# Kernel optimization log

Measured on AMD Instinct MI355X. Metric: run time of the kernel, lower is better.

The kernel has to match this reference:

```python
import jax, jax.numpy as jnp
import numpy as np

B, G, S = 8, 64, 256
DIM = 41           # input_dim = enc_in*2+1
ET = 128           # embed_time = d_model+1
H = 8              # num_heads
EK = ET // H       # per-head time-embed dim
NH = 127           # nhidden = d_model


def setup_inputs() -> dict:
    key = jax.random.key(0)
    ks = jax.random.split(key, 12)
    inp = {
        "query": jax.random.normal(ks[0], (B, G, ET), jnp.float32),
        "key": jax.random.normal(ks[1], (B, S, DIM), jnp.float32),
        "value": jax.random.normal(ks[2], (B, S, DIM), jnp.float32),
        "mask": jax.random.randint(ks[3], (B, S, DIM), 0, 2).astype(jnp.float32),
        "qt": jnp.linspace(0.0, 1.0, G, dtype=jnp.float32),
        "tt": jax.random.uniform(ks[4], (B, S), jnp.float32),
        "stride_in": jnp.zeros((DIM,), jnp.float32),
        # learned params (torch Linear convention: y = x @ W.T + b; we store W already transposed)
        "Wq": jax.random.normal(ks[5], (ET, ET), jnp.float32) / np.sqrt(ET),
        "bq": jnp.zeros((ET,), jnp.float32),
        "Wk": jax.random.normal(ks[6], (DIM, ET), jnp.float32) / np.sqrt(DIM),
        "bk": jnp.zeros((ET,), jnp.float32),
        "Wo": jax.random.normal(ks[7], (DIM * H, NH), jnp.float32) / np.sqrt(DIM * H),
        "bo": jnp.zeros((NH,), jnp.float32),
        "Wr": jax.random.normal(ks[8], (DIM, DIM), jnp.float32) / np.sqrt(DIM),
        "br": jnp.zeros((DIM,), jnp.float32),
    }
    return inp


def reference(query, key, value, mask, qt, tt, stride_in, Wq, bq, Wk, bk, Wo, bo, Wr, br):
    b, s, dim = value.shape
    # per-head projections of time embeddings
    q = (query @ Wq + bq).reshape(b, -1, H, EK).transpose(0, 2, 1, 3)   # [B,H,G,EK]
    k = (key @ Wk + bk).reshape(b, -1, H, EK).transpose(0, 2, 1, 3)     # [B,H,S,EK]
    # per-channel time window half-width: sigmoid(range(stride_list))
    stride = jax.nn.sigmoid(stride_in @ Wr + br)                        # [DIM]
    # time-window mask m[b,g,s,d] = (tt in [qt[g]-stride[d], qt[g]+stride[d]]) & observed
    lo = qt[:, None] - stride[None, :]                                  # [G,DIM]
    hi = qt[:, None] + stride[None, :]                                  # [G,DIM]
    ttd = tt[:, None, :, None]                                          # [B,1,S,1]
    m = (ttd <= hi[None, :, None, :]) & (ttd >= lo[None, :, None, :])   # [B,G,S,DIM]
    m = m & (mask[:, None, :, :] != 0)
    # scaled dot-product scores, broadcast over value dim with per-dim masking
    scores = jnp.einsum('bhge,bhse->bhgs', q, k) / jnp.sqrt(jnp.float32(EK))
    scores = jnp.where(m[:, None], scores[..., None], jnp.float32(-1e9))  # [B,H,G,S,DIM]
    p_attn = jax.nn.softmax(scores, axis=-2)                              # softmax over S
    x = jnp.einsum('bhgsd,bsd->bhgd', p_attn, value)                      # [B,H,G,DIM]
    x = x.transpose(0, 2, 1, 3).reshape(b, -1, H * dim)                   # [B,G,H*DIM]
    out = x @ Wo + bo                                                     # [B,G,NH]
    return out
```

## Files before the change

kernel.cpp:

```cpp
#include <hip/hip_runtime.h>
#include <math.h>

#define B 8
#define G 64
#define S 256
#define DIM 41
#define ET 128
#define H 8
#define EK 16
#define NH 127
#define HD (H*DIM)

__global__ __launch_bounds__(256) void prep_kernel(const float* __restrict__ key,
                                                   const float* __restrict__ Wk,
                                                   const float* __restrict__ bk,
                                                   const float* __restrict__ query,
                                                   const float* __restrict__ Wq,
                                                   const float* __restrict__ bq,
                                                   const float* __restrict__ mask,
                                                   const float* __restrict__ qt,
                                                   const float* __restrict__ tt,
                                                   const float* __restrict__ stride_in,
                                                   const float* __restrict__ Wr,
                                                   const float* __restrict__ br,
                                                   float* __restrict__ kpT,
                                                   float* __restrict__ qp,
                                                   unsigned int* __restrict__ embitsT) {
    const int bid = blockIdx.x;
    const int tid = threadIdx.x;

    if (bid < 1024) {
        __shared__ float klds[2][48];
        const int half = tid >> 7;
        const int j = tid & 127;
        const int row = bid * 2 + half;
        if (j < DIM) klds[half][j] = key[row * DIM + j];
        __syncthreads();
        float acc = bk[j];
#pragma unroll
        for (int i = 0; i < DIM; ++i) acc = fmaf(klds[half][i], Wk[i * ET + j], acc);
        const int b = row >> 8, s = row & 255;
        kpT[b * 32768 + (j >> 2) * 1024 + s * 4 + (j & 3)] = acc;
    } else if (bid < 1280) {
        __shared__ float qlds[2][ET];
        const int base = (bid - 1024) * 2;
        ((float*)qlds)[tid] = query[base * ET + tid];
        __syncthreads();
        const int half = tid >> 7;
        const int j = tid & 127;
        float a0 = 0.f, a1 = 0.f, a2 = 0.f, a3 = 0.f;
#pragma unroll 8
        for (int i = 0; i < ET; i += 4) {
            a0 = fmaf(qlds[half][i + 0], Wq[(i + 0) * ET + j], a0);
            a1 = fmaf(qlds[half][i + 1], Wq[(i + 1) * ET + j], a1);
            a2 = fmaf(qlds[half][i + 2], Wq[(i + 2) * ET + j], a2);
            a3 = fmaf(qlds[half][i + 3], Wq[(i + 3) * ET + j], a3);
        }
        qp[(base + half) * ET + j] = bq[j] + ((a0 + a1) + (a2 + a3));
    } else {
        __shared__ float strd[DIM];
        const int bg = bid - 1280;
        const int b = bg >> 6, g = bg & 63;
        if (tid < DIM) {
            float a = br[tid];
            for (int i = 0; i < DIM; ++i) a = fmaf(stride_in[i], Wr[i * DIM + tid], a);
            strd[tid] = 1.0f / (1.0f + expf(-a));
        }
        const int s = tid;
        const float t = tt[b * S + s];
        const float qtg = qt[g];
        const float* mrow = mask + (size_t)(b * S + s) * DIM;
        unsigned int m0 = 0u, m1 = 0u;
#pragma unroll
        for (int d = 0; d < DIM; ++d) {
            const bool mb = (mrow[d] != 0.0f);
            if (d < 32) m0 |= ((unsigned)mb) << d;
            else        m1 |= ((unsigned)mb) << (d - 32);
        }
        __syncthreads();
        const int w = tid >> 6;
        unsigned int* outp = embitsT + (size_t)bg * (DIM * 8);
#pragma unroll
        for (int d = 0; d < DIM; ++d) {
            const float sd = strd[d];
            const float lo = qtg - sd, hi = qtg + sd;
            const unsigned int mbit = (d < 32) ? ((m0 >> d) & 1u) : ((m1 >> (d - 32)) & 1u);
            const int ok = (t >= lo) & (t <= hi) & (int)mbit;
            const unsigned long long bal = __ballot(ok);
            if ((tid & 63) == 0) {
                outp[d * 8 + 2 * w]     = (unsigned int)bal;
                outp[d * 8 + 2 * w + 1] = (unsigned int)(bal >> 32);
            }
        }
    }
}

__global__ __launch_bounds__(512) void main_kernel(const float* __restrict__ kpT,
                                                   const float* __restrict__ qp,
                                                   const unsigned int* __restrict__ embitsT,
                                                   const float* __restrict__ value,
                                                   const float* __restrict__ Wo,
                                                   const float* __restrict__ bo,
                                                   float* __restrict__ out) {
    __shared__ float se[H][S];
    __shared__ float vlds[S * DIM];
    __shared__ float qv[ET];
    __shared__ float Mb[H];
    __shared__ float xrow[HD];
    __shared__ float po[4][128];

    const int bg = blockIdx.x;
    const int b = bg >> 6;
    const int tid = threadIdx.x;

    const int hd_h = tid / DIM;
    const int hd_d = tid - hd_h * DIM;
    unsigned int ebw0 = 0, ebw1 = 0, ebw2 = 0, ebw3 = 0, ebw4 = 0, ebw5 = 0, ebw6 = 0, ebw7 = 0;
    if (tid < HD) {
        const uint4* p = reinterpret_cast<const uint4*>(embitsT + (size_t)bg * (DIM * 8) + hd_d * 8);
        const uint4 e0 = p[0], e1 = p[1];
        ebw0 = e0.x; ebw1 = e0.y; ebw2 = e0.z; ebw3 = e0.w;
        ebw4 = e1.x; ebw5 = e1.y; ebw6 = e1.z; ebw7 = e1.w;
    }

    if (tid < ET) qv[tid] = qp[(size_t)bg * ET + tid];
    for (int idx = tid; idx < S * DIM; idx += 512) vlds[idx] = value[(size_t)b * S * DIM + idx];
    __syncthreads();

    float sc[H];
    if (tid < S) {
        const int s = tid;
        const float4* kb = reinterpret_cast<const float4*>(kpT) + (size_t)b * 8192 + s;
#pragma unroll
        for (int h = 0; h < H; ++h) {
            float a = 0.f;
#pragma unroll
            for (int e4 = 0; e4 < 4; ++e4) {
                const float4 kv = kb[(h * 4 + e4) * 256];
                a = fmaf(qv[h * EK + e4 * 4 + 0], kv.x, a);
                a = fmaf(qv[h * EK + e4 * 4 + 1], kv.y, a);
                a = fmaf(qv[h * EK + e4 * 4 + 2], kv.z, a);
                a = fmaf(qv[h * EK + e4 * 4 + 3], kv.w, a);
            }
            sc[h] = a * 0.25f;
            se[h][s] = sc[h];
        }
    }
    __syncthreads();

    if (tid < S) {
        const int h = tid >> 5, j = tid & 31;
        float m = se[h][j];
#pragma unroll
        for (int k = 1; k < 8; ++k) m = fmaxf(m, se[h][j + 32 * k]);
#pragma unroll
        for (int off = 16; off; off >>= 1) m = fmaxf(m, __shfl_xor(m, off, 32));
        if (j == 0) Mb[h] = m;
    }
    __syncthreads();

    if (tid < S) {
        const int s = tid;
#pragma unroll
        for (int h = 0; h < H; ++h) se[h][s] = __expf(sc[h] - Mb[h]);
    }
    __syncthreads();

    if (tid < HD) {
        const int h = hd_h, d = hd_d;
        float Ssum = 0.f, acc = 0.f;
        const unsigned int ws[8] = {ebw0, ebw1, ebw2, ebw3, ebw4, ebw5, ebw6, ebw7};
#pragma unroll
        for (int k = 0; k < 8; ++k) {
            const unsigned int wv = ws[k];
#pragma unroll 8
            for (int i = 0; i < 32; ++i) {
                const int s = k * 32 + i;
                const float e = se[h][s];
                const float v = vlds[s * DIM + d];
                const float wgt = ((wv >> i) & 1u) ? e : 0.f;
                Ssum += wgt;
                acc = fmaf(wgt, v, acc);
            }
        }
        float r;
        if (Ssum != 0.f) {
            r = acc / Ssum;
        } else {
            float vs = 0.f;
            for (int s = 0; s < S; ++s) vs += vlds[s * DIM + d];
            r = vs * (1.0f / S);
        }
        xrow[tid] = r;
    }
    __syncthreads();

    {
        const int n = tid & 127, c = tid >> 7;
        if (n < NH) {
            const int i0 = c * 82;
            float a0 = 0.f, a1 = 0.f;
#pragma unroll 2
            for (int i = i0; i < i0 + 82; i += 2) {
                a0 = fmaf(xrow[i],     Wo[(size_t)i * NH + n],       a0);
                a1 = fmaf(xrow[i + 1], Wo[(size_t)(i + 1) * NH + n], a1);
            }
            po[c][n] = a0 + a1;
        }
    }
    __syncthreads();
    if (tid < NH) {
        out[(size_t)bg * NH + tid] = bo[tid] + ((po[0][tid] + po[1][tid]) + (po[2][tid] + po[3][tid]));
    }
}

extern "C" void kernel_launch(void* const* d_in, const int* in_sizes, int n_in,
                              void* d_out, int out_size, void* d_ws, size_t ws_size,
                              hipStream_t stream) {
    const float* query     = (const float*)d_in[0];
    const float* key       = (const float*)d_in[1];
    const float* value     = (const float*)d_in[2];
    const float* mask      = (const float*)d_in[3];
    const float* qt        = (const float*)d_in[4];
    const float* tt        = (const float*)d_in[5];
    const float* stride_in = (const float*)d_in[6];
    const float* Wq        = (const float*)d_in[7];
    const float* bq        = (const float*)d_in[8];
    const float* Wk        = (const float*)d_in[9];
    const float* bk        = (const float*)d_in[10];
    const float* Wo        = (const float*)d_in[11];
    const float* bo        = (const float*)d_in[12];
    const float* Wr        = (const float*)d_in[13];
    const float* br        = (const float*)d_in[14];
    float* out = (float*)d_out;

    float* kpT = (float*)d_ws;
    float* qp = kpT + (size_t)B * H * 4 * S * 4;
    unsigned int* embitsT = (unsigned int*)(qp + (size_t)B * G * ET);

    prep_kernel<<<1792, 256, 0, stream>>>(key, Wk, bk, query, Wq, bq, mask, qt, tt,
                                          stride_in, Wr, br, kpT, qp, embitsT);
    main_kernel<<<B * G, 512, 0, stream>>>(kpT, qp, embitsT, value, Wo, bo, out);
}
```

Baseline: 34.58 us.

## Register-tile masked softmax-value reduction and stage mask loads through shared memory

The main kernel's weighted value reduction changes from one thread per (head,dim) looping over all 256 keys to a register tile. Each thread covers 4 heads by 4 dims over a 16-key chunk, reading float4 from padded value and transposed exp buffers, and the chunks are reduced through shared memory. It also uses wave-level shuffles for the row max, drops the block to 384 threads, and stages the mask through shared memory in the prep kernel so loads coalesce. The aim is more data reuse per shared-memory load and fewer strided global reads, at the cost of more registers, an extra reduction pass, and higher LDS use.

```diff
diff --git a/kernel.cpp b/kernel.cpp
--- a/kernel.cpp
+++ b/kernel.cpp
@@ -10,6 +10,8 @@
 #define EK 16
 #define NH 127
 #define HD (H*DIM)
+#define VROW 44
+#define SEROW 12
 
 __global__ __launch_bounds__(256) void prep_kernel(const float* __restrict__ key,
                                                    const float* __restrict__ Wk,
@@ -26,39 +28,44 @@
                                                    float* __restrict__ kpT,
                                                    float* __restrict__ qp,
                                                    unsigned int* __restrict__ embitsT) {
+    __shared__ float smem[5248 + 64];
     const int bid = blockIdx.x;
     const int tid = threadIdx.x;
 
     if (bid < 1024) {
-        __shared__ float klds[2][48];
+        float* k0 = smem;
+        float* k1 = smem + 48;
         const int half = tid >> 7;
         const int j = tid & 127;
         const int row = bid * 2 + half;
-        if (j < DIM) klds[half][j] = key[row * DIM + j];
+        if (j < DIM) (half ? k1 : k0)[j] = key[row * DIM + j];
         __syncthreads();
+        const float* kr = half ? k1 : k0;
         float acc = bk[j];
 #pragma unroll
-        for (int i = 0; i < DIM; ++i) acc = fmaf(klds[half][i], Wk[i * ET + j], acc);
+        for (int i = 0; i < DIM; ++i) acc = fmaf(kr[i], Wk[i * ET + j], acc);
         const int b = row >> 8, s = row & 255;
         kpT[b * 32768 + (j >> 2) * 1024 + s * 4 + (j & 3)] = acc;
     } else if (bid < 1280) {
-        __shared__ float qlds[2][ET];
+        float* qlds = smem;
         const int base = (bid - 1024) * 2;
-        ((float*)qlds)[tid] = query[base * ET + tid];
+        qlds[tid] = query[base * ET + tid];
         __syncthreads();
         const int half = tid >> 7;
         const int j = tid & 127;
+        const float* qr = qlds + half * 128;
         float a0 = 0.f, a1 = 0.f, a2 = 0.f, a3 = 0.f;
 #pragma unroll 8
         for (int i = 0; i < ET; i += 4) {
-            a0 = fmaf(qlds[half][i + 0], Wq[(i + 0) * ET + j], a0);
-            a1 = fmaf(qlds[half][i + 1], Wq[(i + 1) * ET + j], a1);
-            a2 = fmaf(qlds[half][i + 2], Wq[(i + 2) * ET + j], a2);
-            a3 = fmaf(qlds[half][i + 3], Wq[(i + 3) * ET + j], a3);
+            a0 = fmaf(qr[i + 0], Wq[(i + 0) * ET + j], a0);
+            a1 = fmaf(qr[i + 1], Wq[(i + 1) * ET + j], a1);
+            a2 = fmaf(qr[i + 2], Wq[(i + 2) * ET + j], a2);
+            a3 = fmaf(qr[i + 3], Wq[(i + 3) * ET + j], a3);
         }
         qp[(base + half) * ET + j] = bq[j] + ((a0 + a1) + (a2 + a3));
     } else {
-        __shared__ float strd[DIM];
+        float* mlds = smem;
+        float* strd = smem + 5248;
         const int bg = bid - 1280;
         const int b = bg >> 6, g = bg & 63;
         if (tid < DIM) {
@@ -66,71 +73,81 @@
             for (int i = 0; i < DIM; ++i) a = fmaf(stride_in[i], Wr[i * DIM + tid], a);
             strd[tid] = 1.0f / (1.0f + expf(-a));
         }
-        const int s = tid;
-        const float t = tt[b * S + s];
+        __syncthreads();
         const float qtg = qt[g];
-        const float* mrow = mask + (size_t)(b * S + s) * DIM;
-        unsigned int m0 = 0u, m1 = 0u;
-#pragma unroll
-        for (int d = 0; d < DIM; ++d) {
-            const bool mb = (mrow[d] != 0.0f);
-            if (d < 32) m0 |= ((unsigned)mb) << d;
-            else        m1 |= ((unsigned)mb) << (d - 32);
-        }
-        __syncthreads();
-        const int w = tid >> 6;
-        unsigned int* outp = embitsT + (size_t)bg * (DIM * 8);
-#pragma unroll
-        for (int d = 0; d < DIM; ++d) {
-            const float sd = strd[d];
-            const float lo = qtg - sd, hi = qtg + sd;
-            const unsigned int mbit = (d < 32) ? ((m0 >> d) & 1u) : ((m1 >> (d - 32)) & 1u);
-            const int ok = (t >= lo) & (t <= hi) & (int)mbit;
-            const unsigned long long bal = __ballot(ok);
-            if ((tid & 63) == 0) {
-                outp[d * 8 + 2 * w]     = (unsigned int)bal;
-                outp[d * 8 + 2 * w + 1] = (unsigned int)(bal >> 32);
-            }
+        for (int rr = 0; rr < 2; ++rr) {
+            for (int idx = tid; idx < 5248; idx += 256)
+                mlds[idx] = mask[(size_t)b * S * DIM + rr * 5248 + idx];
+            __syncthreads();
+            if (tid < 128) {
+                const int s = rr * 128 + tid;
+                const float t = tt[b * S + s];
+                const int wv = tid >> 6;
+                const int w = rr * 2 + wv;
+                unsigned int* op = embitsT + (size_t)bg * (DIM * 8) + w * 2;
+#pragma unroll
+                for (int d = 0; d < DIM; ++d) {
+                    const float sd = strd[d];
+                    const int ok = (t >= qtg - sd) & (t <= qtg + sd) & (mlds[tid * DIM + d] != 0.0f);
+                    const unsigned long long bal = __ballot(ok);
+                    if ((tid & 63) == 0) {
+                        op[d * 8 + 0] = (unsigned int)bal;
+                        op[d * 8 + 1] = (unsigned int)(bal >> 32);
+                    }
+                }
+            }
+            __syncthreads();
         }
     }
 }
 
-__global__ __launch_bounds__(512) void main_kernel(const float* __restrict__ kpT,
+__global__ __launch_bounds__(384) void main_kernel(const float* __restrict__ kpT,
                                                    const float* __restrict__ qp,
                                                    const unsigned int* __restrict__ embitsT,
                                                    const float* __restrict__ value,
                                                    const float* __restrict__ Wo,
                                                    const float* __restrict__ bo,
                                                    float* __restrict__ out) {
-    __shared__ float se[H][S];
-    __shared__ float vlds[S * DIM];
+    __shared__ float vbuf[S * VROW];
+    __shared__ float seT[S][SEROW];
     __shared__ float qv[ET];
-    __shared__ float Mb[H];
     __shared__ float xrow[HD];
-    __shared__ float po[4][128];
+    __shared__ float po[3][128];
+    __shared__ float wmax[4][8];
+    __shared__ float Mb[8];
 
     const int bg = blockIdx.x;
     const int b = bg >> 6;
     const int tid = threadIdx.x;
 
-    const int hd_h = tid / DIM;
-    const int hd_d = tid - hd_h * DIM;
-    unsigned int ebw0 = 0, ebw1 = 0, ebw2 = 0, ebw3 = 0, ebw4 = 0, ebw5 = 0, ebw6 = 0, ebw7 = 0;
-    if (tid < HD) {
-        const uint4* p = reinterpret_cast<const uint4*>(embitsT + (size_t)bg * (DIM * 8) + hd_d * 8);
-        const uint4 e0 = p[0], e1 = p[1];
-        ebw0 = e0.x; ebw1 = e0.y; ebw2 = e0.z; ebw3 = e0.w;
-        ebw4 = e1.x; ebw5 = e1.y; ebw6 = e1.z; ebw7 = e1.w;
+    const int hh = tid / 176;
+    const int rem = tid - hh * 176;
+    const int sc = rem / 11;
+    const int d4 = rem - sc * 11;
+    unsigned int wd0 = 0, wd1 = 0, wd2 = 0, wd3 = 0;
+    if (tid < 352) {
+        const unsigned int* eb = embitsT + (size_t)bg * (DIM * 8) + (sc >> 1);
+        const int d0 = d4 * 4;
+        wd0 = (d0 + 0 < DIM) ? eb[(d0 + 0) * 8] : 0u;
+        wd1 = (d0 + 1 < DIM) ? eb[(d0 + 1) * 8] : 0u;
+        wd2 = (d0 + 2 < DIM) ? eb[(d0 + 2) * 8] : 0u;
+        wd3 = (d0 + 3 < DIM) ? eb[(d0 + 3) * 8] : 0u;
     }
 
     if (tid < ET) qv[tid] = qp[(size_t)bg * ET + tid];
-    for (int idx = tid; idx < S * DIM; idx += 512) vlds[idx] = value[(size_t)b * S * DIM + idx];
-    __syncthreads();
-
-    float sc[H];
+    for (int q = tid; q < S * 11; q += 384) {
+        const int s = q / 11, dq = q - (q / 11) * 11;
+        const float* vp = value + (size_t)b * S * DIM + s * DIM + dq * 4;
+        float4 t;
+        if (dq < 10) { t.x = vp[0]; t.y = vp[1]; t.z = vp[2]; t.w = vp[3]; }
+        else         { t.x = vp[0]; t.y = 0.f;   t.z = 0.f;   t.w = 0.f;  }
+        *reinterpret_cast<float4*>(&vbuf[s * VROW + dq * 4]) = t;
+    }
+    __syncthreads();
+
+    float sc8[H];
     if (tid < S) {
-        const int s = tid;
-        const float4* kb = reinterpret_cast<const float4*>(kpT) + (size_t)b * 8192 + s;
+        const float4* kb = reinterpret_cast<const float4*>(kpT) + (size_t)b * 8192 + tid;
 #pragma unroll
         for (int h = 0; h < H; ++h) {
             float a = 0.f;
@@ -142,53 +159,93 @@
                 a = fmaf(qv[h * EK + e4 * 4 + 2], kv.z, a);
                 a = fmaf(qv[h * EK + e4 * 4 + 3], kv.w, a);
             }
-            sc[h] = a * 0.25f;
-            se[h][s] = sc[h];
-        }
-    }
-    __syncthreads();
-
+            sc8[h] = a * 0.25f;
+        }
+#pragma unroll
+        for (int h = 0; h < H; ++h) {
+            float m = sc8[h];
+#pragma unroll
+            for (int off = 32; off; off >>= 1) m = fmaxf(m, __shfl_xor(m, off));
+            if ((tid & 63) == 0) wmax[tid >> 6][h] = m;
+        }
+    }
+    __syncthreads();
+    if (tid < H) Mb[tid] = fmaxf(fmaxf(wmax[0][tid], wmax[1][tid]),
+                                 fmaxf(wmax[2][tid], wmax[3][tid]));
+    __syncthreads();
     if (tid < S) {
-        const int h = tid >> 5, j = tid & 31;
-        float m = se[h][j];
-#pragma unroll
-        for (int k = 1; k < 8; ++k) m = fmaxf(m, se[h][j + 32 * k]);
-#pragma unroll
-        for (int off = 16; off; off >>= 1) m = fmaxf(m, __shfl_xor(m, off, 32));
-        if (j == 0) Mb[h] = m;
-    }
-    __syncthreads();
-
-    if (tid < S) {
-        const int s = tid;
-#pragma unroll
-        for (int h = 0; h < H; ++h) se[h][s] = __expf(sc[h] - Mb[h]);
+        float4 e0, e1;
+        e0.x = __expf(sc8[0] - Mb[0]); e0.y = __expf(sc8[1] - Mb[1]);
+        e0.z = __expf(sc8[2] - Mb[2]); e0.w = __expf(sc8[3] - Mb[3]);
+        e1.x = __expf(sc8[4] - Mb[4]); e1.y = __expf(sc8[5] - Mb[5]);
+        e1.z = __expf(sc8[6] - Mb[6]); e1.w = __expf(sc8[7] - Mb[7]);
+        *reinterpret_cast<float4*>(&seT[tid][0]) = e0;
+        *reinterpret_cast<float4*>(&seT[tid][4]) = e1;
+    }
+    __syncthreads();
+
+    float aS[4][4] = {{0.f}};
+    float aA[4][4] = {{0.f}};
+    if (tid < 352) {
+        const int sbase = sc * 16;
+        const int shift0 = (sc & 1) * 16;
+#pragma unroll
+        for (int i = 0; i < 16; ++i) {
+            const int s = sbase + i;
+            const float4 v = *reinterpret_cast<const float4*>(&vbuf[s * VROW + d4 * 4]);
+            const float4 e = *reinterpret_cast<const float4*>(&seT[s][hh * 4]);
+            const unsigned sh = shift0 + i;
+            const float b0 = ((wd0 >> sh) & 1u) ? 1.f : 0.f;
+            const float b1 = ((wd1 >> sh) & 1u) ? 1.f : 0.f;
+            const float b2 = ((wd2 >> sh) & 1u) ? 1.f : 0.f;
+            const float b3 = ((wd3 >> sh) & 1u) ? 1.f : 0.f;
+            const float vm0 = v.x * b0, vm1 = v.y * b1, vm2 = v.z * b2, vm3 = v.w * b3;
+            const float ee[4] = {e.x, e.y, e.z, e.w};
+#pragma unroll
+            for (int a = 0; a < 4; ++a) {
+                aA[a][0] = fmaf(ee[a], vm0, aA[a][0]);
+                aA[a][1] = fmaf(ee[a], vm1, aA[a][1]);
+                aA[a][2] = fmaf(ee[a], vm2, aA[a][2]);
+                aA[a][3] = fmaf(ee[a], vm3, aA[a][3]);
+                aS[a][0] = fmaf(ee[a], b0, aS[a][0]);
+                aS[a][1] = fmaf(ee[a], b1, aS[a][1]);
+                aS[a][2] = fmaf(ee[a], b2, aS[a][2]);
+                aS[a][3] = fmaf(ee[a], b3, aS[a][3]);
+            }
+        }
+    }
+    __syncthreads();
+
+    float* pS = vbuf;
+    float* pA = vbuf + 328 * 17;
+    if (tid < 352) {
+#pragma unroll
+        for (int a = 0; a < 4; ++a) {
+#pragma unroll
+            for (int j = 0; j < 4; ++j) {
+                const int d = d4 * 4 + j;
+                if (d < DIM) {
+                    const int hd = (hh * 4 + a) * DIM + d;
+                    pS[hd * 17 + sc] = aS[a][j];
+                    pA[hd * 17 + sc] = aA[a][j];
+                }
+            }
+        }
     }
     __syncthreads();
 
     if (tid < HD) {
-        const int h = hd_h, d = hd_d;
-        float Ssum = 0.f, acc = 0.f;
-        const unsigned int ws[8] = {ebw0, ebw1, ebw2, ebw3, ebw4, ebw5, ebw6, ebw7};
-#pragma unroll
-        for (int k = 0; k < 8; ++k) {
-            const unsigned int wv = ws[k];
-#pragma unroll 8
-            for (int i = 0; i < 32; ++i) {
-                const int s = k * 32 + i;
-                const float e = se[h][s];
-                const float v = vlds[s * DIM + d];
-                const float wgt = ((wv >> i) & 1u) ? e : 0.f;
-                Ssum += wgt;
-                acc = fmaf(wgt, v, acc);
-            }
-        }
+        float Ss = 0.f, Aa = 0.f;
+#pragma unroll
+        for (int k = 0; k < 16; ++k) { Ss += pS[tid * 17 + k]; Aa += pA[tid * 17 + k]; }
         float r;
-        if (Ssum != 0.f) {
-            r = acc / Ssum;
+        if (Ss != 0.f) {
+            r = Aa / Ss;
         } else {
+            const int d = tid % DIM;
             float vs = 0.f;
-            for (int s = 0; s < S; ++s) vs += vlds[s * DIM + d];
+            const float* vc = value + (size_t)b * S * DIM + d;
+            for (int s2 = 0; s2 < S; ++s2) vs += vc[(size_t)s2 * DIM];
             r = vs * (1.0f / S);
         }
         xrow[tid] = r;
@@ -197,11 +254,10 @@
 
     {
         const int n = tid & 127, c = tid >> 7;
+        const int i0 = c * 110, i1 = (c == 2) ? HD : (i0 + 110);
         if (n < NH) {
-            const int i0 = c * 82;
             float a0 = 0.f, a1 = 0.f;
-#pragma unroll 2
-            for (int i = i0; i < i0 + 82; i += 2) {
+            for (int i = i0; i < i1; i += 2) {
                 a0 = fmaf(xrow[i],     Wo[(size_t)i * NH + n],       a0);
                 a1 = fmaf(xrow[i + 1], Wo[(size_t)(i + 1) * NH + n], a1);
             }
@@ -209,9 +265,8 @@
         }
     }
     __syncthreads();
-    if (tid < NH) {
-        out[(size_t)bg * NH + tid] = bo[tid] + ((po[0][tid] + po[1][tid]) + (po[2][tid] + po[3][tid]));
-    }
+    if (tid < NH)
+        out[(size_t)bg * NH + tid] = bo[tid] + ((po[0][tid] + po[1][tid]) + po[2][tid]);
 }
 
 extern "C" void kernel_launch(void* const* d_in, const int* in_sizes, int n_in,
@@ -240,5 +295,5 @@
 
     prep_kernel<<<1792, 256, 0, stream>>>(key, Wk, bk, query, Wq, bq, mask, qt, tt,
                                           stride_in, Wr, br, kpT, qp, embitsT);
-    main_kernel<<<B * G, 512, 0, stream>>>(kpT, qp, embitsT, value, Wo, bo, out);
+    main_kernel<<<B * G, 384, 0, stream>>>(kpT, qp, embitsT, value, Wo, bo, out);
 }
```

Measured after the change: 52.42 us. +51.6%, slower.

## Transpose value in prep kernel and vectorize masked weighted sum via float4 LDS reads

Applied to the files above, without the earlier changes.

Adds prep blocks that write a transposed copy of value ([B,DIM,S]) to the workspace. The main kernel stages it into padded LDS rows so each thread can read four consecutive s values of both exp-scores and values as float4, replacing strided scalar LDS reads in the hot weighted-sum loop. The mask-bit blocks now stage mask rows through shared memory in two halves for coalesced global loads. The cost is an extra global round-trip for value, more shared memory in prep blocks, and half the threads idle during mask ballot.

```diff
diff --git a/kernel.cpp b/kernel.cpp
--- a/kernel.cpp
+++ b/kernel.cpp
@@ -10,6 +10,7 @@
 #define EK 16
 #define NH 127
 #define HD (H*DIM)
+#define VTROW 260
 
 __global__ __launch_bounds__(256) void prep_kernel(const float* __restrict__ key,
                                                    const float* __restrict__ Wk,
@@ -23,42 +24,49 @@
                                                    const float* __restrict__ stride_in,
                                                    const float* __restrict__ Wr,
                                                    const float* __restrict__ br,
+                                                   const float* __restrict__ value,
                                                    float* __restrict__ kpT,
                                                    float* __restrict__ qp,
-                                                   unsigned int* __restrict__ embitsT) {
+                                                   unsigned int* __restrict__ embitsT,
+                                                   float* __restrict__ vTg) {
+    __shared__ float smem[5248 + 64];
     const int bid = blockIdx.x;
     const int tid = threadIdx.x;
 
     if (bid < 1024) {
-        __shared__ float klds[2][48];
+        float* k0 = smem;
+        float* k1 = smem + 48;
         const int half = tid >> 7;
         const int j = tid & 127;
         const int row = bid * 2 + half;
-        if (j < DIM) klds[half][j] = key[row * DIM + j];
+        if (j < DIM) (half ? k1 : k0)[j] = key[row * DIM + j];
         __syncthreads();
+        const float* kr = half ? k1 : k0;
         float acc = bk[j];
 #pragma unroll
-        for (int i = 0; i < DIM; ++i) acc = fmaf(klds[half][i], Wk[i * ET + j], acc);
+        for (int i = 0; i < DIM; ++i) acc = fmaf(kr[i], Wk[i * ET + j], acc);
         const int b = row >> 8, s = row & 255;
         kpT[b * 32768 + (j >> 2) * 1024 + s * 4 + (j & 3)] = acc;
     } else if (bid < 1280) {
-        __shared__ float qlds[2][ET];
+        float* qlds = smem;
         const int base = (bid - 1024) * 2;
-        ((float*)qlds)[tid] = query[base * ET + tid];
+        qlds[tid] = query[base * ET + tid];
         __syncthreads();
         const int half = tid >> 7;
         const int j = tid & 127;
+        const float* qr = qlds + half * 128;
         float a0 = 0.f, a1 = 0.f, a2 = 0.f, a3 = 0.f;
 #pragma unroll 8
         for (int i = 0; i < ET; i += 4) {
-            a0 = fmaf(qlds[half][i + 0], Wq[(i + 0) * ET + j], a0);
-            a1 = fmaf(qlds[half][i + 1], Wq[(i + 1) * ET + j], a1);
-            a2 = fmaf(qlds[half][i + 2], Wq[(i + 2) * ET + j], a2);
-            a3 = fmaf(qlds[half][i + 3], Wq[(i + 3) * ET + j], a3);
+            a0 = fmaf(qr[i + 0], Wq[(i + 0) * ET + j], a0);
+            a1 = fmaf(qr[i + 1], Wq[(i + 1) * ET + j], a1);
+            a2 = fmaf(qr[i + 2], Wq[(i + 2) * ET + j], a2);
+            a3 = fmaf(qr[i + 3], Wq[(i + 3) * ET + j], a3);
         }
         qp[(base + half) * ET + j] = bq[j] + ((a0 + a1) + (a2 + a3));
-    } else {
-        __shared__ float strd[DIM];
+    } else if (bid < 1792) {
+        float* mlds = smem;
+        float* strd = smem + 5248;
         const int bg = bid - 1280;
         const int b = bg >> 6, g = bg & 63;
         if (tid < DIM) {
@@ -66,31 +74,36 @@
             for (int i = 0; i < DIM; ++i) a = fmaf(stride_in[i], Wr[i * DIM + tid], a);
             strd[tid] = 1.0f / (1.0f + expf(-a));
         }
-        const int s = tid;
-        const float t = tt[b * S + s];
+        __syncthreads();
         const float qtg = qt[g];
-        const float* mrow = mask + (size_t)(b * S + s) * DIM;
-        unsigned int m0 = 0u, m1 = 0u;
-#pragma unroll
-        for (int d = 0; d < DIM; ++d) {
-            const bool mb = (mrow[d] != 0.0f);
-            if (d < 32) m0 |= ((unsigned)mb) << d;
-            else        m1 |= ((unsigned)mb) << (d - 32);
-        }
-        __syncthreads();
-        const int w = tid >> 6;
-        unsigned int* outp = embitsT + (size_t)bg * (DIM * 8);
-#pragma unroll
-        for (int d = 0; d < DIM; ++d) {
-            const float sd = strd[d];
-            const float lo = qtg - sd, hi = qtg + sd;
-            const unsigned int mbit = (d < 32) ? ((m0 >> d) & 1u) : ((m1 >> (d - 32)) & 1u);
-            const int ok = (t >= lo) & (t <= hi) & (int)mbit;
-            const unsigned long long bal = __ballot(ok);
-            if ((tid & 63) == 0) {
-                outp[d * 8 + 2 * w]     = (unsigned int)bal;
-                outp[d * 8 + 2 * w + 1] = (unsigned int)(bal >> 32);
-            }
+        for (int rr = 0; rr < 2; ++rr) {
+            for (int idx = tid; idx < 5248; idx += 256)
+                mlds[idx] = mask[(size_t)b * S * DIM + rr * 5248 + idx];
+            __syncthreads();
+            if (tid < 128) {
+                const int s = rr * 128 + tid;
+                const float t = tt[b * S + s];
+                const int wv = tid >> 6;
+                const int w = rr * 2 + wv;
+                unsigned int* op = embitsT + (size_t)bg * (DIM * 8) + w * 2;
+#pragma unroll
+                for (int d = 0; d < DIM; ++d) {
+                    const float sd = strd[d];
+                    const int ok = (t >= qtg - sd) & (t <= qtg + sd) & (mlds[tid * DIM + d] != 0.0f);
+                    const unsigned long long bal = __ballot(ok);
+                    if ((tid & 63) == 0) {
+                        op[d * 8 + 0] = (unsigned int)bal;
+                        op[d * 8 + 1] = (unsigned int)(bal >> 32);
+                    }
+                }
+            }
+            __syncthreads();
+        }
+    } else {
+        const int b = bid - 1792;
+        for (int idx = tid; idx < DIM * S; idx += 256) {
+            const int d = idx >> 8, s = idx & 255;
+            vTg[(size_t)b * (DIM * S) + idx] = value[(size_t)b * S * DIM + s * DIM + d];
         }
     }
 }
@@ -98,12 +111,12 @@
 __global__ __launch_bounds__(512) void main_kernel(const float* __restrict__ kpT,
                                                    const float* __restrict__ qp,
                                                    const unsigned int* __restrict__ embitsT,
-                                                   const float* __restrict__ value,
+                                                   const float* __restrict__ vTg,
                                                    const float* __restrict__ Wo,
                                                    const float* __restrict__ bo,
                                                    float* __restrict__ out) {
+    __shared__ float vT[DIM * VTROW];
     __shared__ float se[H][S];
-    __shared__ float vlds[S * DIM];
     __shared__ float qv[ET];
     __shared__ float Mb[H];
     __shared__ float xrow[HD];
@@ -124,13 +137,15 @@
     }
 
     if (tid < ET) qv[tid] = qp[(size_t)bg * ET + tid];
-    for (int idx = tid; idx < S * DIM; idx += 512) vlds[idx] = value[(size_t)b * S * DIM + idx];
-    __syncthreads();
-
-    float sc[H];
+    for (int idx = tid; idx < DIM * S; idx += 512) {
+        const int d = idx >> 8, s = idx & 255;
+        vT[d * VTROW + s] = vTg[(size_t)b * (DIM * S) + idx];
+    }
+    __syncthreads();
+
+    float sc8[H];
     if (tid < S) {
-        const int s = tid;
-        const float4* kb = reinterpret_cast<const float4*>(kpT) + (size_t)b * 8192 + s;
+        const float4* kb = reinterpret_cast<const float4*>(kpT) + (size_t)b * 8192 + tid;
 #pragma unroll
         for (int h = 0; h < H; ++h) {
             float a = 0.f;
@@ -142,8 +157,8 @@
                 a = fmaf(qv[h * EK + e4 * 4 + 2], kv.z, a);
                 a = fmaf(qv[h * EK + e4 * 4 + 3], kv.w, a);
             }
-            sc[h] = a * 0.25f;
-            se[h][s] = sc[h];
+            sc8[h] = a * 0.25f;
+            se[h][tid] = sc8[h];
         }
     }
     __syncthreads();
@@ -160,27 +175,35 @@
     __syncthreads();
 
     if (tid < S) {
-        const int s = tid;
-#pragma unroll
-        for (int h = 0; h < H; ++h) se[h][s] = __expf(sc[h] - Mb[h]);
+#pragma unroll
+        for (int h = 0; h < H; ++h) se[h][tid] = __expf(sc8[h] - Mb[h]);
     }
     __syncthreads();
 
     if (tid < HD) {
         const int h = hd_h, d = hd_d;
+        const float* erow = &se[h][0];
+        const float* vrow = &vT[d * VTROW];
+        const unsigned int ws[8] = {ebw0, ebw1, ebw2, ebw3, ebw4, ebw5, ebw6, ebw7};
         float Ssum = 0.f, acc = 0.f;
-        const unsigned int ws[8] = {ebw0, ebw1, ebw2, ebw3, ebw4, ebw5, ebw6, ebw7};
 #pragma unroll
         for (int k = 0; k < 8; ++k) {
             const unsigned int wv = ws[k];
-#pragma unroll 8
-            for (int i = 0; i < 32; ++i) {
-                const int s = k * 32 + i;
-                const float e = se[h][s];
-                const float v = vlds[s * DIM + d];
-                const float wgt = ((wv >> i) & 1u) ? e : 0.f;
-                Ssum += wgt;
-                acc = fmaf(wgt, v, acc);
+#pragma unroll
+            for (int q = 0; q < 8; ++q) {
+                const int s0 = k * 32 + q * 4;
+                const float4 e4 = *reinterpret_cast<const float4*>(&erow[s0]);
+                const float4 v4 = *reinterpret_cast<const float4*>(&vrow[s0]);
+                const unsigned sh = q * 4;
+                const float em0 = ((wv >> (sh + 0)) & 1u) ? e4.x : 0.f;
+                const float em1 = ((wv >> (sh + 1)) & 1u) ? e4.y : 0.f;
+                const float em2 = ((wv >> (sh + 2)) & 1u) ? e4.z : 0.f;
+                const float em3 = ((wv >> (sh + 3)) & 1u) ? e4.w : 0.f;
+                Ssum += em0 + em1 + em2 + em3;
+                acc = fmaf(em0, v4.x, acc);
+                acc = fmaf(em1, v4.y, acc);
+                acc = fmaf(em2, v4.z, acc);
+                acc = fmaf(em3, v4.w, acc);
             }
         }
         float r;
@@ -188,7 +211,7 @@
             r = acc / Ssum;
         } else {
             float vs = 0.f;
-            for (int s = 0; s < S; ++s) vs += vlds[s * DIM + d];
+            for (int s2 = 0; s2 < S; ++s2) vs += vrow[s2];
             r = vs * (1.0f / S);
         }
         xrow[tid] = r;
@@ -209,9 +232,8 @@
         }
     }
     __syncthreads();
-    if (tid < NH) {
+    if (tid < NH)
         out[(size_t)bg * NH + tid] = bo[tid] + ((po[0][tid] + po[1][tid]) + (po[2][tid] + po[3][tid]));
-    }
 }
 
 extern "C" void kernel_launch(void* const* d_in, const int* in_sizes, int n_in,
@@ -237,8 +259,9 @@
     float* kpT = (float*)d_ws;
     float* qp = kpT + (size_t)B * H * 4 * S * 4;
     unsigned int* embitsT = (unsigned int*)(qp + (size_t)B * G * ET);
-
-    prep_kernel<<<1792, 256, 0, stream>>>(key, Wk, bk, query, Wq, bq, mask, qt, tt,
-                                          stride_in, Wr, br, kpT, qp, embitsT);
-    main_kernel<<<B * G, 512, 0, stream>>>(kpT, qp, embitsT, value, Wo, bo, out);
+    float* vTg = (float*)(embitsT + (size_t)B * G * DIM * 8);
+
+    prep_kernel<<<1800, 256, 0, stream>>>(key, Wk, bk, query, Wq, bq, mask, qt, tt,
+                                          stride_in, Wr, br, value, kpT, qp, embitsT, vTg);
+    main_kernel<<<B * G, 512, 0, stream>>>(kpT, qp, embitsT, vTg, Wo, bo, out);
 }
```

Result: slower. 66.53 us (+92.4%).
